# Optimization experiments

Measured on AMD Instinct MI355X. Metric: run time of the kernel, lower is better.

## Reference

```python
import jax, jax.numpy as jnp
import numpy as np

N = 100000        # num nodes
E = 800000        # num edges
N_T = 1
IN_FEATS = 128
NUM_HEAD = 8
O_FEATS = 16
O_HEAD = NUM_HEAD * O_FEATS  # 128
LN_EPS = 1e-5


def setup_inputs() -> dict:
    key = jax.random.key(0)
    ks = [jax.random.fold_in(key, i) for i in range(16)]
    feats = jax.random.normal(ks[0], (N, N_T, IN_FEATS), dtype=jnp.float32)
    edge_src = jax.random.randint(ks[1], (E,), 0, N, dtype=jnp.int32)
    # ensure every node has at least one incoming edge (avoids 0/0 in wv/z)
    dst_rest = jax.random.randint(ks[2], (E - N,), 0, N, dtype=jnp.int32)
    edge_dst = jax.random.permutation(ks[3], jnp.concatenate([jnp.arange(N, dtype=jnp.int32), dst_rest]))
    s_in = 1.0 / np.sqrt(IN_FEATS)
    s_oh = 1.0 / np.sqrt(O_HEAD)
    Wq = jax.random.normal(ks[4], (IN_FEATS, O_HEAD), dtype=jnp.float32) * s_in
    bq = jnp.zeros((O_HEAD,), dtype=jnp.float32)
    Wk = jax.random.normal(ks[5], (IN_FEATS, O_HEAD), dtype=jnp.float32) * s_in
    bk = jnp.zeros((O_HEAD,), dtype=jnp.float32)
    Wv = jax.random.normal(ks[6], (IN_FEATS, O_HEAD), dtype=jnp.float32) * s_in
    bv = jnp.zeros((O_HEAD,), dtype=jnp.float32)
    Wo = jax.random.normal(ks[7], (O_HEAD, O_HEAD), dtype=jnp.float32) * s_oh
    bo = jnp.zeros((O_HEAD,), dtype=jnp.float32)
    Wffn = jax.random.normal(ks[8], (IN_FEATS, O_HEAD), dtype=jnp.float32) * s_in
    bffn = jnp.zeros((O_HEAD,), dtype=jnp.float32)
    ln_g = jnp.ones((O_HEAD,), dtype=jnp.float32)
    ln_b = jnp.zeros((O_HEAD,), dtype=jnp.float32)
    return {"feats": feats, "edge_src": edge_src, "edge_dst": edge_dst,
            "Wq": Wq, "bq": bq, "Wk": Wk, "bk": bk, "Wv": Wv, "bv": bv,
            "Wo": Wo, "bo": bo, "Wffn": Wffn, "bffn": bffn,
            "ln_g": ln_g, "ln_b": ln_b}


def _layer_norm(x, g, b):
    mu = jnp.mean(x, axis=-1, keepdims=True)
    var = jnp.mean(jnp.square(x - mu), axis=-1, keepdims=True)
    return (x - mu) * jax.lax.rsqrt(var + LN_EPS) * g + b


def reference(feats, edge_src, edge_dst, Wq, bq, Wk, bk, Wv, bv, Wo, bo, Wffn, bffn, ln_g, ln_b):
    n = feats.shape[0]
    # q/k/v projections: [N, n_T, H, D]
    q = (feats @ Wq + bq).reshape(n, N_T, NUM_HEAD, O_FEATS)
    k = (feats @ Wk + bk).reshape(n, N_T, NUM_HEAD, O_FEATS)
    v = (feats @ Wv + bv).reshape(n, N_T, NUM_HEAD, O_FEATS)
    # edge scores: src k . dst q, scaled, clamped exp  -> [E, n_T, H, 1]
    score = jnp.sum(k[edge_src] * q[edge_dst], axis=-1, keepdims=True)
    score = jnp.exp(jnp.clip(score / np.sqrt(IN_FEATS), -5.0, 5.0))
    # segment sums to destination nodes
    wv = jax.ops.segment_sum(v[edge_src] * score, edge_dst, num_segments=n)
    z = jax.ops.segment_sum(score, edge_dst, num_segments=n)
    wv = wv / z                                   # [N, n_T, H, D]
    o = wv.reshape(n, N_T, O_HEAD) @ Wo + bo      # output projection
    h = (feats @ Wffn + bffn) + o                 # FFN skip + attention out
    h = h + _layer_norm(h, ln_g, ln_b)
    return h
```

## Files before the change

kernel.cpp:

```cpp
#include <hip/hip_runtime.h>
#include <hip/hip_bf16.h>

#define N_NODES 100000
#define N_EDGES 800000
#define CAP     64

typedef unsigned short u16;
typedef unsigned int   u32;
typedef __attribute__((ext_vector_type(8))) short bf16x8;
typedef __attribute__((ext_vector_type(4))) float f32x4;

__device__ inline u32 pack_bf2(float a, float b) {
    __hip_bfloat16 ha = __float2bfloat16(a), hb = __float2bfloat16(b);
    u16 ua, ub;
    __builtin_memcpy(&ua, &ha, 2);
    __builtin_memcpy(&ub, &hb, 2);
    return (u32)ua | ((u32)ub << 16);
}
__device__ inline u16 to_bf16(float a) {
    __hip_bfloat16 h = __float2bfloat16(a);
    u16 u; __builtin_memcpy(&u, &h, 2);
    return u;
}
__device__ inline void unpk(u32 w, float& a, float& b) {
    a = __uint_as_float(w << 16);
    b = __uint_as_float(w & 0xffff0000u);
}

__global__ __launch_bounds__(256) void prep_weights(
    const float* __restrict__ Wq, const float* __restrict__ Wk,
    const float* __restrict__ Wv, const float* __restrict__ Wf,
    const float* __restrict__ Wo, u16* __restrict__ WcatT, u16* __restrict__ WoT)
{
    int idx = blockIdx.x * 256 + threadIdx.x;
    if (idx < 512 * 128) {
        int n = idx >> 7, kk = idx & 127;
        const float* W = (n < 128) ? Wq : (n < 256) ? Wk : (n < 384) ? Wv : Wf;
        WcatT[idx] = to_bf16(W[kk * 128 + (n & 127)]);
    } else if (idx < 512 * 128 + 128 * 128) {
        int i2 = idx - 512 * 128;
        int n = i2 >> 7, kk = i2 & 127;
        WoT[i2] = to_bf16(Wo[kk * 128 + n]);
    }
}

__global__ __launch_bounds__(384) void proj_mfma(
    const float* __restrict__ feats, const u16* __restrict__ WT,
    const float* __restrict__ bq, const float* __restrict__ bk,
    const float* __restrict__ bv,
    u16* __restrict__ q, u16* __restrict__ k, u16* __restrict__ v)
{
    __shared__ __align__(16) u16 As[64][136];
    const int tid  = threadIdx.x;
    const int row0 = blockIdx.x * 64;

    #pragma unroll
    for (int i = 0; i < 3; ++i) {
        int idx = tid + i * 384;
        if (idx < 1024) {
            int r = idx >> 4, c8 = (idx & 15) * 8;
            int gr = row0 + r;
            float4 f0, f1;
            if (gr < N_NODES) {
                const float4* p = reinterpret_cast<const float4*>(feats + (size_t)gr * 128 + c8);
                f0 = p[0]; f1 = p[1];
            } else {
                f0 = make_float4(0.f,0.f,0.f,0.f); f1 = f0;
            }
            uint4 pk;
            pk.x = pack_bf2(f0.x, f0.y); pk.y = pack_bf2(f0.z, f0.w);
            pk.z = pack_bf2(f1.x, f1.y); pk.w = pack_bf2(f1.z, f1.w);
            *reinterpret_cast<uint4*>(&As[r][c8]) = pk;
        }
    }
    __syncthreads();

    const int wid = tid >> 6, l = tid & 63;
    const int q4 = l >> 4, c16 = l & 15;
    const int colg0 = wid * 64;

    f32x4 acc[4][4];
    #pragma unroll
    for (int a = 0; a < 4; ++a)
        #pragma unroll
        for (int b = 0; b < 4; ++b)
            acc[a][b] = (f32x4){0.f,0.f,0.f,0.f};

    #pragma unroll
    for (int ks = 0; ks < 4; ++ks) {
        const int k0 = ks * 32 + q4 * 8;
        bf16x8 afr[4], bfr[4];
        #pragma unroll
        for (int mt = 0; mt < 4; ++mt)
            afr[mt] = *reinterpret_cast<const bf16x8*>(&As[mt * 16 + c16][k0]);
        #pragma unroll
        for (int nt = 0; nt < 4; ++nt)
            bfr[nt] = *reinterpret_cast<const bf16x8*>(WT + (size_t)(colg0 + nt * 16 + c16) * 128 + k0);
        #pragma unroll
        for (int mt = 0; mt < 4; ++mt)
            #pragma unroll
            for (int nt = 0; nt < 4; ++nt)
                acc[mt][nt] = __builtin_amdgcn_mfma_f32_16x16x32_bf16(afr[mt], bfr[nt], acc[mt][nt], 0, 0, 0);
    }

    const float* bias_src = (wid < 2) ? bq : (wid < 4) ? bk : bv;
    u16* outb = (wid < 2) ? q : (wid < 4) ? k : v;
    const int cbase = colg0 - (wid >> 1) * 128;

    #pragma unroll
    for (int nt = 0; nt < 4; ++nt) {
        const int col = cbase + nt * 16 + c16;
        const float bias = bias_src[col];
        #pragma unroll
        for (int mt = 0; mt < 4; ++mt) {
            #pragma unroll
            for (int j = 0; j < 4; ++j) {
                int gr = row0 + mt * 16 + q4 * 4 + j;
                if (gr >= N_NODES) continue;
                outb[(size_t)gr * 128 + col] = to_bf16(acc[mt][nt][j] + bias);
            }
        }
    }
}

__global__ __launch_bounds__(256) void bucket_kernel(
    const int* __restrict__ esrc, const int* __restrict__ edst,
    int* __restrict__ cnt, int* __restrict__ bucket)
{
    int e = blockIdx.x * 256 + threadIdx.x;
    if (e >= N_EDGES) return;
    int d = edst[e];
    int pos = atomicAdd(&cnt[d], 1);
    if (pos < CAP) bucket[(size_t)d * CAP + pos] = esrc[e];
}

__global__ __launch_bounds__(256) void agg_fused(
    const u16* __restrict__ q, const u16* __restrict__ k, const u16* __restrict__ v,
    const int* __restrict__ cnt, const int* __restrict__ bucket,
    u16* __restrict__ wv)
{
    const int wid  = threadIdx.x >> 6;
    const int lane = threadIdx.x & 63;
    const int node = blockIdx.x * 4 + wid;
    int deg = cnt[node]; if (deg > CAP) deg = CAP;

    const int grp = lane >> 3;
    const int el  = lane & 7;

    const float scale = 0.08838834764831845f;
    const uint4* qp = reinterpret_cast<const uint4*>(q + (size_t)node * 128 + el * 16);
    uint4 q0 = qp[0], q1 = qp[1];
    float qf[16];
    {
        u32 qw[8] = {q0.x,q0.y,q0.z,q0.w,q1.x,q1.y,q1.z,q1.w};
        #pragma unroll
        for (int j = 0; j < 8; ++j) {
            float a, b; unpk(qw[j], a, b);
            qf[2*j] = a * scale; qf[2*j+1] = b * scale;
        }
    }

    int srcs = (lane < deg) ? bucket[(size_t)node * CAP + lane] : 0;

    float acc[16];
    #pragma unroll
    for (int j = 0; j < 16; ++j) acc[j] = 0.f;
    float z = 0.f;

    const int nIter = (deg + 7) >> 3;
    for (int it = 0; it < nIter; ++it) {
        int i = it * 8 + grp;
        bool valid = (i < deg);
        int s = __shfl(srcs, i);
        const uint4* kp = reinterpret_cast<const uint4*>(k + (size_t)s * 128 + el * 16);
        uint4 k0 = kp[0], k1 = kp[1];
        const uint4* vp = reinterpret_cast<const uint4*>(v + (size_t)s * 128 + el * 16);
        uint4 v0 = vp[0], v1 = vp[1];

        u32 kw[8] = {k0.x,k0.y,k0.z,k0.w,k1.x,k1.y,k1.z,k1.w};
        float p = 0.f;
        #pragma unroll
        for (int j = 0; j < 8; ++j) {
            float a, b; unpk(kw[j], a, b);
            p = fmaf(a, qf[2*j], p);
            p = fmaf(b, qf[2*j+1], p);
        }
        p = fminf(fmaxf(p, -5.f), 5.f);
        float sc = valid ? __expf(p) : 0.f;

        u32 vw[8] = {v0.x,v0.y,v0.z,v0.w,v1.x,v1.y,v1.z,v1.w};
        #pragma unroll
        for (int j = 0; j < 8; ++j) {
            float a, b; unpk(vw[j], a, b);
            acc[2*j]   = fmaf(a, sc, acc[2*j]);
            acc[2*j+1] = fmaf(b, sc, acc[2*j+1]);
        }
        z += sc;
    }

    #pragma unroll
    for (int mask = 8; mask <= 32; mask <<= 1) {
        #pragma unroll
        for (int j = 0; j < 16; ++j) acc[j] += __shfl_xor(acc[j], mask);
        z += __shfl_xor(z, mask);
    }

    if (grp == 0) {
        float inv = 1.f / z;
        uint4 w0, w1;
        w0.x = pack_bf2(acc[0]*inv,  acc[1]*inv);
        w0.y = pack_bf2(acc[2]*inv,  acc[3]*inv);
        w0.z = pack_bf2(acc[4]*inv,  acc[5]*inv);
        w0.w = pack_bf2(acc[6]*inv,  acc[7]*inv);
        w1.x = pack_bf2(acc[8]*inv,  acc[9]*inv);
        w1.y = pack_bf2(acc[10]*inv, acc[11]*inv);
        w1.z = pack_bf2(acc[12]*inv, acc[13]*inv);
        w1.w = pack_bf2(acc[14]*inv, acc[15]*inv);
        uint4* wp = reinterpret_cast<uint4*>(wv + (size_t)node * 128 + el * 16);
        wp[0] = w0; wp[1] = w1;
    }
}

__global__ __launch_bounds__(256) void out_mfma(
    const float* __restrict__ feats, const u16* __restrict__ wv,
    const u16* __restrict__ WoT, const u16* __restrict__ WcatT,
    const float* __restrict__ bo, const float* __restrict__ bffn,
    const float* __restrict__ lg, const float* __restrict__ lb,
    float* __restrict__ out)
{
    __shared__ __align__(16) char smem[2 * 64 * 136 * sizeof(u16)];
    u16 (*Awv)[136] = reinterpret_cast<u16(*)[136]>(smem);
    u16 (*Aft)[136] = reinterpret_cast<u16(*)[136]>(smem + 64 * 136 * sizeof(u16));
    float (*Hs)[132] = reinterpret_cast<float(*)[132]>(smem);

    const int tid  = threadIdx.x;
    const int row0 = blockIdx.x * 64;
    const u16* WfT = WcatT + 384 * 128;

    #pragma unroll
    for (int i = 0; i < 4; ++i) {
        int idx = tid + i * 256;
        int r = idx >> 4, c8 = (idx & 15) * 8;
        int gr = row0 + r; if (gr >= N_NODES) gr = N_NODES - 1;
        *reinterpret_cast<uint4*>(&Awv[r][c8]) =
            *reinterpret_cast<const uint4*>(wv + (size_t)gr * 128 + c8);
        const float4* p = reinterpret_cast<const float4*>(feats + (size_t)gr * 128 + c8);
        float4 f0 = p[0], f1 = p[1];
        uint4 pk;
        pk.x = pack_bf2(f0.x, f0.y); pk.y = pack_bf2(f0.z, f0.w);
        pk.z = pack_bf2(f1.x, f1.y); pk.w = pack_bf2(f1.z, f1.w);
        *reinterpret_cast<uint4*>(&Aft[r][c8]) = pk;
    }
    __syncthreads();

    const int wid = tid >> 6, l = tid & 63;
    const int q4 = l >> 4, c16 = l & 15;
    const int col0 = wid * 32;

    f32x4 acc[4][2];
    #pragma unroll
    for (int a = 0; a < 4; ++a) { acc[a][0] = (f32x4){0.f,0.f,0.f,0.f}; acc[a][1] = acc[a][0]; }

    #pragma unroll
    for (int ks = 0; ks < 4; ++ks) {
        const int k0 = ks * 32 + q4 * 8;
        bf16x8 afr[4], bfr[2];
        #pragma unroll
        for (int mt = 0; mt < 4; ++mt)
            afr[mt] = *reinterpret_cast<const bf16x8*>(&Awv[mt * 16 + c16][k0]);
        #pragma unroll
        for (int nt = 0; nt < 2; ++nt)
            bfr[nt] = *reinterpret_cast<const bf16x8*>(WoT + (size_t)(col0 + nt * 16 + c16) * 128 + k0);
        #pragma unroll
        for (int mt = 0; mt < 4; ++mt)
            #pragma unroll
            for (int nt = 0; nt < 2; ++nt)
                acc[mt][nt] = __builtin_amdgcn_mfma_f32_16x16x32_bf16(afr[mt], bfr[nt], acc[mt][nt], 0, 0, 0);
    }
    #pragma unroll
    for (int ks = 0; ks < 4; ++ks) {
        const int k0 = ks * 32 + q4 * 8;
        bf16x8 afr[4], bfr[2];
        #pragma unroll
        for (int mt = 0; mt < 4; ++mt)
            afr[mt] = *reinterpret_cast<const bf16x8*>(&Aft[mt * 16 + c16][k0]);
        #pragma unroll
        for (int nt = 0; nt < 2; ++nt)
            bfr[nt] = *reinterpret_cast<const bf16x8*>(WfT + (size_t)(col0 + nt * 16 + c16) * 128 + k0);
        #pragma unroll
        for (int mt = 0; mt < 4; ++mt)
            #pragma unroll
            for (int nt = 0; nt < 2; ++nt)
                acc[mt][nt] = __builtin_amdgcn_mfma_f32_16x16x32_bf16(afr[mt], bfr[nt], acc[mt][nt], 0, 0, 0);
    }
    __syncthreads();

    #pragma unroll
    for (int nt = 0; nt < 2; ++nt) {
        const int col = col0 + nt * 16 + c16;
        const float bias = bo[col] + bffn[col];
        #pragma unroll
        for (int mt = 0; mt < 4; ++mt) {
            #pragma unroll
            for (int j = 0; j < 4; ++j) {
                int r = mt * 16 + q4 * 4 + j;
                Hs[r][col] = acc[mt][nt][j] + bias;
            }
        }
    }
    __syncthreads();

    const int r   = tid >> 2;
    const int sub = tid & 3;
    float sum = 0.f, sq = 0.f;
    #pragma unroll
    for (int jj = 0; jj < 8; ++jj) {
        float4 x = *reinterpret_cast<const float4*>(&Hs[r][(sub + jj * 4) * 4]);
        sum += x.x + x.y + x.z + x.w;
        sq  += x.x*x.x + x.y*x.y + x.z*x.z + x.w*x.w;
    }
    sum += __shfl_xor(sum, 1); sq += __shfl_xor(sq, 1);
    sum += __shfl_xor(sum, 2); sq += __shfl_xor(sq, 2);
    float mu   = sum * (1.f / 128.f);
    float var  = sq * (1.f / 128.f) - mu * mu;
    float rsig = rsqrtf(var + 1e-5f);

    int gr = row0 + r;
    if (gr < N_NODES) {
        #pragma unroll
        for (int jj = 0; jj < 8; ++jj) {
            int c = (sub + jj * 4) * 4;
            float4 x = *reinterpret_cast<const float4*>(&Hs[r][c]);
            float4 g = *reinterpret_cast<const float4*>(lg + c);
            float4 b = *reinterpret_cast<const float4*>(lb + c);
            float4 o;
            o.x = x.x + (x.x - mu) * rsig * g.x + b.x;
            o.y = x.y + (x.y - mu) * rsig * g.y + b.y;
            o.z = x.z + (x.z - mu) * rsig * g.z + b.z;
            o.w = x.w + (x.w - mu) * rsig * g.w + b.w;
            *reinterpret_cast<float4*>(out + (size_t)gr * 128 + c) = o;
        }
    }
}

extern "C" void kernel_launch(void* const* d_in, const int* in_sizes, int n_in,
                              void* d_out, int out_size, void* d_ws, size_t ws_size,
                              hipStream_t stream) {
    const float* feats = (const float*)d_in[0];
    const int*   esrc  = (const int*)d_in[1];
    const int*   edst  = (const int*)d_in[2];
    const float* Wq = (const float*)d_in[3];  const float* bq = (const float*)d_in[4];
    const float* Wk = (const float*)d_in[5];  const float* bk = (const float*)d_in[6];
    const float* Wv = (const float*)d_in[7];  const float* bv = (const float*)d_in[8];
    const float* Wo = (const float*)d_in[9];  const float* bo = (const float*)d_in[10];
    const float* Wf = (const float*)d_in[11]; const float* bf = (const float*)d_in[12];
    const float* lg = (const float*)d_in[13]; const float* lb = (const float*)d_in[14];
    float* out = (float*)d_out;

    char* ws = (char*)d_ws;
    const size_t NB = (size_t)N_NODES * 128 * sizeof(u16);
    u16* q     = (u16*)(ws);
    u16* k     = (u16*)(ws + NB);
    u16* v     = (u16*)(ws + 2 * NB);
    u16* wv    = (u16*)(ws + 3 * NB);
    u16* WcatT = (u16*)(ws + 4 * NB);
    u16* WoT   = (u16*)(ws + 4 * NB + 512 * 128 * sizeof(u16));
    int* cnt   = (int*)(ws + 4 * NB + (512 * 128 + 128 * 128) * sizeof(u16));
    int* bucket= (int*)(ws + 4 * NB + (512 * 128 + 128 * 128) * sizeof(u16)
                             + (size_t)N_NODES * sizeof(int));

    hipMemsetAsync(cnt, 0, (size_t)N_NODES * sizeof(int), stream);

    prep_weights<<<320, 256, 0, stream>>>(Wq, Wk, Wv, Wf, Wo, WcatT, WoT);
    proj_mfma<<<(N_NODES + 63) / 64, 384, 0, stream>>>(feats, WcatT, bq, bk, bv,
                                                       q, k, v);
    bucket_kernel<<<(N_EDGES + 255) / 256, 256, 0, stream>>>(esrc, edst, cnt, bucket);
    agg_fused<<<N_NODES / 4, 256, 0, stream>>>(q, k, v, cnt, bucket, wv);
    out_mfma<<<(N_NODES + 63) / 64, 256, 0, stream>>>(feats, wv, WoT, WcatT,
                                                      bo, bf, lg, lb, out);
}
```

Measured before the change: 239.7 us.

## Make projection kernel persistent with register-resident weights and vectorized stores

The QKV projection kernel becomes a grid-stride persistent kernel with 521 blocks. Each wave loads its weight fragments into registers once and reuses them across many 64-row tiles, instead of reloading them from global memory for every tile. The MFMA operands are swapped so each lane holds four consecutive output columns, which allows packed 8-byte bf16 stores and float4 bias loads in place of scalar 2-byte stores. In exchange it uses more registers (launch bounds ask for 3 blocks per CU), adds an extra barrier per tile, and gives up the overlap between tiles' loads that separate blocks provided.

```diff
diff --git a/kernel.cpp b/kernel.cpp
--- a/kernel.cpp
+++ b/kernel.cpp
@@ -4,6 +4,7 @@
 #define N_NODES 100000
 #define N_EDGES 800000
 #define CAP     64
+#define NTILES  ((N_NODES + 63) / 64)
 
 typedef unsigned short u16;
 typedef unsigned int   u32;
@@ -44,82 +45,92 @@
     }
 }
 
-__global__ __launch_bounds__(384) void proj_mfma(
+__global__ __launch_bounds__(384, 3) void proj_mfma(
     const float* __restrict__ feats, const u16* __restrict__ WT,
     const float* __restrict__ bq, const float* __restrict__ bk,
     const float* __restrict__ bv,
     u16* __restrict__ q, u16* __restrict__ k, u16* __restrict__ v)
 {
     __shared__ __align__(16) u16 As[64][136];
-    const int tid  = threadIdx.x;
-    const int row0 = blockIdx.x * 64;
-
-    #pragma unroll
-    for (int i = 0; i < 3; ++i) {
-        int idx = tid + i * 384;
-        if (idx < 1024) {
-            int r = idx >> 4, c8 = (idx & 15) * 8;
-            int gr = row0 + r;
-            float4 f0, f1;
-            if (gr < N_NODES) {
-                const float4* p = reinterpret_cast<const float4*>(feats + (size_t)gr * 128 + c8);
-                f0 = p[0]; f1 = p[1];
-            } else {
-                f0 = make_float4(0.f,0.f,0.f,0.f); f1 = f0;
-            }
-            uint4 pk;
-            pk.x = pack_bf2(f0.x, f0.y); pk.y = pack_bf2(f0.z, f0.w);
-            pk.z = pack_bf2(f1.x, f1.y); pk.w = pack_bf2(f1.z, f1.w);
-            *reinterpret_cast<uint4*>(&As[r][c8]) = pk;
-        }
-    }
-    __syncthreads();
-
+    const int tid = threadIdx.x;
     const int wid = tid >> 6, l = tid & 63;
     const int q4 = l >> 4, c16 = l & 15;
     const int colg0 = wid * 64;
 
-    f32x4 acc[4][4];
-    #pragma unroll
-    for (int a = 0; a < 4; ++a)
-        #pragma unroll
-        for (int b = 0; b < 4; ++b)
-            acc[a][b] = (f32x4){0.f,0.f,0.f,0.f};
-
-    #pragma unroll
-    for (int ks = 0; ks < 4; ++ks) {
-        const int k0 = ks * 32 + q4 * 8;
-        bf16x8 afr[4], bfr[4];
-        #pragma unroll
-        for (int mt = 0; mt < 4; ++mt)
-            afr[mt] = *reinterpret_cast<const bf16x8*>(&As[mt * 16 + c16][k0]);
+    bf16x8 wfr[4][4];
+    #pragma unroll
+    for (int ks = 0; ks < 4; ++ks)
         #pragma unroll
         for (int nt = 0; nt < 4; ++nt)
-            bfr[nt] = *reinterpret_cast<const bf16x8*>(WT + (size_t)(colg0 + nt * 16 + c16) * 128 + k0);
-        #pragma unroll
-        for (int mt = 0; mt < 4; ++mt)
-            #pragma unroll
-            for (int nt = 0; nt < 4; ++nt)
-                acc[mt][nt] = __builtin_amdgcn_mfma_f32_16x16x32_bf16(afr[mt], bfr[nt], acc[mt][nt], 0, 0, 0);
-    }
+            wfr[ks][nt] = *reinterpret_cast<const bf16x8*>(
+                WT + (size_t)(colg0 + nt * 16 + c16) * 128 + ks * 32 + q4 * 8);
 
     const float* bias_src = (wid < 2) ? bq : (wid < 4) ? bk : bv;
     u16* outb = (wid < 2) ? q : (wid < 4) ? k : v;
     const int cbase = colg0 - (wid >> 1) * 128;
 
-    #pragma unroll
-    for (int nt = 0; nt < 4; ++nt) {
-        const int col = cbase + nt * 16 + c16;
-        const float bias = bias_src[col];
-        #pragma unroll
-        for (int mt = 0; mt < 4; ++mt) {
-            #pragma unroll
-            for (int j = 0; j < 4; ++j) {
-                int gr = row0 + mt * 16 + q4 * 4 + j;
-                if (gr >= N_NODES) continue;
-                outb[(size_t)gr * 128 + col] = to_bf16(acc[mt][nt][j] + bias);
+    for (int tile = blockIdx.x; tile < NTILES; tile += gridDim.x) {
+        const int row0 = tile * 64;
+
+        #pragma unroll
+        for (int i = 0; i < 3; ++i) {
+            int idx = tid + i * 384;
+            if (idx < 1024) {
+                int r = idx >> 4, c8 = (idx & 15) * 8;
+                int gr = row0 + r;
+                float4 f0, f1;
+                if (gr < N_NODES) {
+                    const float4* p = reinterpret_cast<const float4*>(feats + (size_t)gr * 128 + c8);
+                    f0 = p[0]; f1 = p[1];
+                } else {
+                    f0 = make_float4(0.f,0.f,0.f,0.f); f1 = f0;
+                }
+                uint4 pk;
+                pk.x = pack_bf2(f0.x, f0.y); pk.y = pack_bf2(f0.z, f0.w);
+                pk.z = pack_bf2(f1.x, f1.y); pk.w = pack_bf2(f1.z, f1.w);
+                *reinterpret_cast<uint4*>(&As[r][c8]) = pk;
             }
         }
+        __syncthreads();
+
+        f32x4 acc[4][4];
+        #pragma unroll
+        for (int a = 0; a < 4; ++a)
+            #pragma unroll
+            for (int b = 0; b < 4; ++b)
+                acc[a][b] = (f32x4){0.f,0.f,0.f,0.f};
+
+        #pragma unroll
+        for (int ks = 0; ks < 4; ++ks) {
+            const int k0 = ks * 32 + q4 * 8;
+            bf16x8 afr[4];
+            #pragma unroll
+            for (int mt = 0; mt < 4; ++mt)
+                afr[mt] = *reinterpret_cast<const bf16x8*>(&As[mt * 16 + c16][k0]);
+            #pragma unroll
+            for (int mt = 0; mt < 4; ++mt)
+                #pragma unroll
+                for (int nt = 0; nt < 4; ++nt)
+                    acc[mt][nt] = __builtin_amdgcn_mfma_f32_16x16x32_bf16(
+                        wfr[ks][nt], afr[mt], acc[mt][nt], 0, 0, 0);
+        }
+
+        #pragma unroll
+        for (int nt = 0; nt < 4; ++nt) {
+            const int c = cbase + nt * 16 + q4 * 4;
+            float4 b4 = *reinterpret_cast<const float4*>(bias_src + c);
+            #pragma unroll
+            for (int mt = 0; mt < 4; ++mt) {
+                int gr = row0 + mt * 16 + c16;
+                if (gr < N_NODES) {
+                    uint2 pk;
+                    pk.x = pack_bf2(acc[mt][nt][0] + b4.x, acc[mt][nt][1] + b4.y);
+                    pk.y = pack_bf2(acc[mt][nt][2] + b4.z, acc[mt][nt][3] + b4.w);
+                    *reinterpret_cast<uint2*>(outb + (size_t)gr * 128 + c) = pk;
+                }
+            }
+        }
+        __syncthreads();
     }
 }
 
@@ -372,8 +383,7 @@
     hipMemsetAsync(cnt, 0, (size_t)N_NODES * sizeof(int), stream);
 
     prep_weights<<<320, 256, 0, stream>>>(Wq, Wk, Wv, Wf, Wo, WcatT, WoT);
-    proj_mfma<<<(N_NODES + 63) / 64, 384, 0, stream>>>(feats, WcatT, bq, bk, bv,
-                                                       q, k, v);
+    proj_mfma<<<521, 384, 0, stream>>>(feats, WcatT, bq, bk, bv, q, k, v);
     bucket_kernel<<<(N_EDGES + 255) / 256, 256, 0, stream>>>(esrc, edst, cnt, bucket);
     agg_fused<<<N_NODES / 4, 256, 0, stream>>>(q, k, v, cnt, bucket, wv);
     out_mfma<<<(N_NODES + 63) / 64, 256, 0, stream>>>(feats, wv, WoT, WcatT,
```

Measured after the change: 220.0 us. -8.2%, faster.
